# Kernel tuning notes

Measured on AMD Instinct MI355X. Metric: run time of the kernel, lower is better.

The kernel has to match this reference:

```python
import jax, jax.numpy as jnp
import numpy as np

N_NODES = 10000
N_EDGES = 640000
D = 128
BN_EPS = 1e-5


def setup_inputs() -> dict:
    key = jax.random.key(0)
    k1, k2, k3 = jax.random.split(key, 3)
    x = jax.random.normal(k1, (N_NODES, D), dtype=jnp.float32)
    edge_index = jax.random.randint(k2, (2, N_EDGES), 0, N_NODES, dtype=jnp.int64)
    W = jax.random.normal(k3, (D, D), dtype=jnp.float32) * (1.0 / np.sqrt(D))
    b = jnp.zeros((D,), dtype=jnp.float32)
    gamma = jnp.ones((D,), dtype=jnp.float32)
    beta = jnp.zeros((D,), dtype=jnp.float32)
    return {"x": x, "edge_index": edge_index, "W": W, "b": b, "gamma": gamma, "beta": beta}


def reference(x, edge_index, W, b, gamma, beta):
    # GINConv: out_i = MLP((1+eps)*x_i + sum_{j->i} x_j), eps=0
    src = edge_index[0]
    dst = edge_index[1]
    agg = jax.ops.segment_sum(x[src], dst, num_segments=N_NODES)  # [N, D]
    h = agg + x  # (1 + eps) * x with eps = 0
    # MLP inside GINConv: Linear + ReLU
    h = jnp.maximum(h @ W + b, 0.0)
    # outer F.relu (idempotent after inner ReLU, kept for faithfulness)
    h = jnp.maximum(h, 0.0)
    # BatchNorm1d, training-mode batch statistics (biased variance)
    mean = jnp.mean(h, axis=0)
    var = jnp.var(h, axis=0)
    h = (h - mean) * jax.lax.rsqrt(var + BN_EPS) * gamma + beta
    # Dropout in eval mode -> identity. his_x = [h]; return the main output.
    return h
```

## Files before the change

### kernel.cpp

```cpp
#include <hip/hip_runtime.h>

#define N_NODES 10000
#define N_EDGES 640000
#define D 128
#define BN_EPS 1e-5f
#define CAP 128
#define NSTRIPE 16
#define RPB 8
#define NB 1250
#define NBC 157
#define BCAPC 4608
#define ABLK 256
#define ASLICE 2500
#define CSENT 1250

typedef _Float16 half8_t __attribute__((ext_vector_type(8)));
typedef float f32x4 __attribute__((ext_vector_type(4)));
typedef unsigned short u16;

__global__ __launch_bounds__(256) void k_bin(
    const int* __restrict__ ei,
    const float4* __restrict__ x4,
    int* cur,
    int* __restrict__ recs,
    half8_t* __restrict__ xh)
{
    __shared__ int cnt[NBC];
    __shared__ int base_[NBC];
    __shared__ int loff[NBC];
    __shared__ int sc[256];
    __shared__ int sorted[ASLICE];
    const int b = blockIdx.x, t = threadIdx.x;

    {
        const int n8 = N_NODES * D / 8;
        for (int i = b * 256 + t; i < n8; i += ABLK * 256) {
            const float4 a = x4[2 * i];
            const float4 c = x4[2 * i + 1];
            half8_t h;
            h[0] = (_Float16)a.x; h[1] = (_Float16)a.y;
            h[2] = (_Float16)a.z; h[3] = (_Float16)a.w;
            h[4] = (_Float16)c.x; h[5] = (_Float16)c.y;
            h[6] = (_Float16)c.z; h[7] = (_Float16)c.w;
            xh[i] = h;
        }
    }

    if (t < NBC) cnt[t] = 0;
    __syncthreads();

    const int e0 = b * ASLICE;
    for (int i = t; i < ASLICE; i += 256)
        atomicAdd(&cnt[ei[N_EDGES + e0 + i] >> 6], 1);
    __syncthreads();

    sc[t] = (t < NBC) ? cnt[t] : 0;
    __syncthreads();
    #pragma unroll
    for (int off = 1; off < 256; off <<= 1) {
        const int add = (t >= off) ? sc[t - off] : 0;
        __syncthreads();
        sc[t] += add;
        __syncthreads();
    }

    const unsigned cbase = (unsigned)cur[CSENT];
    if (t < NBC) {
        loff[t]  = sc[t] - cnt[t];
        base_[t] = (int)((unsigned)atomicAdd(&cur[t], cnt[t]) - cbase);
        cnt[t]   = 0;
    }
    __syncthreads();

    for (int i = t; i < ASLICE; i += 256) {
        const int e = e0 + i;
        const int d = ei[N_EDGES + e];
        const int s = ei[e];
        const int bin = d >> 6;
        const int p = atomicAdd(&cnt[bin], 1);
        sorted[loff[bin] + p] = (s << 6) | (d & 63);
    }
    __syncthreads();

    const int g = t >> 4, sl = t & 15;
    for (int bin = g; bin < NBC; bin += 16) {
        const int c  = cnt[bin];
        const int gb = base_[bin];
        const int lo = loff[bin];
        for (int k = sl; k < c; k += 16) {
            const int pos = gb + k;
            if (pos < BCAPC) recs[bin * BCAPC + pos] = sorted[lo + k];
        }
    }
}

__global__ __launch_bounds__(256) void k_gfill(
    const float* __restrict__ x,
    const half8_t* __restrict__ xh8,
    const int* __restrict__ cur,
    const int* __restrict__ recs,
    const float* __restrict__ W,
    const float* __restrict__ bias,
    float* __restrict__ out,
    float* __restrict__ stats)
{
    __shared__ u16 lst[RPB * CAP];
    __shared__ int cnt[RPB];
    __shared__ float hs[RPB][D];
    const int tid  = threadIdx.x;
    const int bin  = blockIdx.x;
    const int cb   = bin >> 3;
    const int sub  = bin & 7;
    const int wv   = tid >> 6;
    const int lane = tid & 63;
    const int qq   = lane >> 4;
    const int l    = lane & 15;
    const float4* __restrict__ x4 = (const float4*)x;

    if (tid < RPB) cnt[tid] = 0;
    __syncthreads();

    const unsigned cbase = (unsigned)cur[CSENT];
    int nrec = (int)((unsigned)cur[cb] - cbase);
    if (nrec > BCAPC) nrec = BCAPC;
    const int* __restrict__ br = recs + cb * BCAPC;
    for (int i = tid; i < nrec; i += 256) {
        const int r = br[i];
        if (((r >> 3) & 7) == sub) {
            const int p = atomicAdd(&cnt[r & 7], 1);
            if (p < CAP) lst[(r & 7) * CAP + p] = (u16)(r >> 6);
        }
    }
    __syncthreads();

    #pragma unroll
    for (int j = 0; j < 2; j++) {
        const int lrow = wv * 2 + j;
        const int node = bin * RPB + lrow;
        int n = cnt[lrow];
        if (n > CAP) n = CAP;
        const u16* __restrict__ myl = &lst[lrow * CAP];
        float acc[8];
        #pragma unroll
        for (int z = 0; z < 8; z++) acc[z] = 0.f;

        int i = 0;
        for (; i + 64 <= n; i += 64) {
            const int sj = (int)myl[i + lane];
            #pragma unroll
            for (int b = 0; b < 2; b++) {
                half8_t v[8];
                #pragma unroll
                for (int u = 0; u < 8; u++) {
                    const int s = __shfl(sj, 4 * (b * 8 + u) + qq, 64);
                    v[u] = xh8[(size_t)s * 16 + l];
                }
                #pragma unroll
                for (int u = 0; u < 8; u++)
                    #pragma unroll
                    for (int z = 0; z < 8; z++)
                        acc[z] += (float)v[u][z];
            }
        }
        const int c = n - i;
        if (c > 0) {
            const int sj = (lane < c) ? (int)myl[i + lane] : 0;
            const int quads = c >> 2;
            for (int t2 = 0; t2 < quads; t2 += 8) {
                half8_t v[8];
                #pragma unroll
                for (int u = 0; u < 8; u++) {
                    const int s = __shfl(sj, (4 * (t2 + u) + qq) & 63, 64);
                    v[u] = xh8[(size_t)s * 16 + l];
                }
                #pragma unroll
                for (int u = 0; u < 8; u++) {
                    if (t2 + u < quads) {
                        #pragma unroll
                        for (int z = 0; z < 8; z++)
                            acc[z] += (float)v[u][z];
                    }
                }
            }
            const int r = c & 3;
            if (r > 0) {
                const int s = __shfl(sj, (4 * quads + qq) & 63, 64);
                const half8_t vv = xh8[(size_t)s * 16 + l];
                if (qq < r) {
                    #pragma unroll
                    for (int z = 0; z < 8; z++)
                        acc[z] += (float)vv[z];
                }
            }
        }
        #pragma unroll
        for (int z = 0; z < 8; z++) {
            acc[z] += __shfl_xor(acc[z], 16, 64);
            acc[z] += __shfl_xor(acc[z], 32, 64);
        }
        if (qq == 0) {
            const float4 xa = x4[(size_t)node * 32 + 2 * l];
            const float4 xb = x4[(size_t)node * 32 + 2 * l + 1];
            *(float4*)&hs[lrow][8 * l] =
                make_float4(acc[0] + xa.x, acc[1] + xa.y, acc[2] + xa.z, acc[3] + xa.w);
            *(float4*)&hs[lrow][8 * l + 4] =
                make_float4(acc[4] + xb.x, acc[5] + xb.y, acc[6] + xb.z, acc[7] + xb.w);
        }
    }
    __syncthreads();

    const int col = tid & 127;
    const int rg  = tid >> 7;
    float a[4] = {0.f, 0.f, 0.f, 0.f};
    #pragma unroll 8
    for (int k = 0; k < D; k++) {
        const float w = W[k * D + col];
        #pragma unroll
        for (int r = 0; r < 4; r++)
            a[r] = fmaf(hs[rg * 4 + r][k], w, a[r]);
    }

    const float bcol = bias[col];
    float s1 = 0.f, s2 = 0.f;
    #pragma unroll
    for (int r = 0; r < 4; r++) {
        const float v = fmaxf(a[r] + bcol, 0.f);
        __builtin_nontemporal_store(v, &out[(size_t)(bin * RPB + rg * 4 + r) * D + col]);
        s1 += v;
        s2 += v * v;
    }

    __syncthreads();
    float* red = &hs[0][0];
    red[tid]       = s1;
    red[256 + tid] = s2;
    __syncthreads();
    if (tid < D) {
        float* sp = &stats[(size_t)(bin & (NSTRIPE - 1)) * 256];
        atomicAdd(&sp[tid],     red[tid]       + red[tid + 128]);
        atomicAdd(&sp[D + tid], red[256 + tid] + red[256 + tid + 128]);
    }
}

__global__ __launch_bounds__(256) void k_bn(
    float* out,
    const float* __restrict__ stats,
    const float* __restrict__ gamma,
    const float* __restrict__ beta)
{
    __shared__ float sc[D], sh[D];
    const int tid = threadIdx.x;
    if (tid < D) {
        const float fbase = stats[NSTRIPE * 256];
        float s = 0.f, q = 0.f;
        #pragma unroll
        for (int cp = 0; cp < NSTRIPE; cp++) {
            s += stats[cp * 256 + tid]     - fbase;
            q += stats[cp * 256 + D + tid] - fbase;
        }
        const float mean = s * (1.0f / N_NODES);
        const float var  = q * (1.0f / N_NODES) - mean * mean;
        const float scale = gamma[tid] * rsqrtf(var + BN_EPS);
        sc[tid] = scale;
        sh[tid] = beta[tid] - mean * scale;
    }
    __syncthreads();

    f32x4* o4 = (f32x4*)out;
    #pragma unroll
    for (int j = 0; j < 2; j++) {
        const int f = blockIdx.x * 512 + j * 256 + tid;
        const int c = (f & 31) << 2;
        f32x4 v = __builtin_nontemporal_load(&o4[f]);
        v.x = v.x * sc[c]     + sh[c];
        v.y = v.y * sc[c + 1] + sh[c + 1];
        v.z = v.z * sc[c + 2] + sh[c + 2];
        v.w = v.w * sc[c + 3] + sh[c + 3];
        __builtin_nontemporal_store(v, &o4[f]);
    }
}

extern "C" void kernel_launch(void* const* d_in, const int* in_sizes, int n_in,
                              void* d_out, int out_size, void* d_ws, size_t ws_size,
                              hipStream_t stream)
{
    const float* x     = (const float*)d_in[0];
    const int*   ei    = (const int*)d_in[1];
    const float* W     = (const float*)d_in[2];
    const float* bias  = (const float*)d_in[3];
    const float* gamma = (const float*)d_in[4];
    const float* beta  = (const float*)d_in[5];
    float* out = (float*)d_out;

    float*   stats = (float*)d_ws;
    int*     cur   = (int*)(stats + NSTRIPE * 256 + 8);
    int*     recs  = cur + 1280;
    half8_t* xh    = (half8_t*)(recs + NBC * BCAPC);

    k_bin<<<ABLK, 256, 0, stream>>>(ei, (const float4*)x, cur, recs, xh);
    k_gfill<<<NB, 256, 0, stream>>>(x, xh, cur, recs, W, bias, out, stats);
    k_bn<<<N_NODES * D / 2048, 256, 0, stream>>>(out, stats, gamma, beta);
}
```

Baseline: 116.6 us.

## Replace global atomic bin cursors with fixed per-block record slots

The binning kernel no longer reserves space in each destination bin with a global atomicAdd on a shared cursor. Each (bin, source block) pair now writes into its own fixed-size slot and stores its count in a separate counts array. The gather kernel then has each of its 256 threads walk one source block's slot for its bin, instead of striding over one contiguous per-bin list. This removes contended global atomics and the cursor sentinel bookkeeping. In exchange, each slot is capped at 48 records, so an unusually dense bin from one slice would silently drop edges, and the per-thread serial slot reads are less coalesced.

New measurement: 166.9 us. +43.1%, slower.

```diff
diff --git a/kernel.cpp b/kernel.cpp
--- a/kernel.cpp
+++ b/kernel.cpp
@@ -9,10 +9,10 @@
 #define RPB 8
 #define NB 1250
 #define NBC 157
-#define BCAPC 4608
+#define SLOT 48
+#define CNTP 160
 #define ABLK 256
 #define ASLICE 2500
-#define CSENT 1250
 
 typedef _Float16 half8_t __attribute__((ext_vector_type(8)));
 typedef float f32x4 __attribute__((ext_vector_type(4)));
@@ -21,12 +21,11 @@
 __global__ __launch_bounds__(256) void k_bin(
     const int* __restrict__ ei,
     const float4* __restrict__ x4,
-    int* cur,
     int* __restrict__ recs,
+    int* __restrict__ cnts,
     half8_t* __restrict__ xh)
 {
     __shared__ int cnt[NBC];
-    __shared__ int base_[NBC];
     __shared__ int loff[NBC];
     __shared__ int sc[256];
     __shared__ int sorted[ASLICE];
@@ -64,12 +63,7 @@
         __syncthreads();
     }
 
-    const unsigned cbase = (unsigned)cur[CSENT];
-    if (t < NBC) {
-        loff[t]  = sc[t] - cnt[t];
-        base_[t] = (int)((unsigned)atomicAdd(&cur[t], cnt[t]) - cbase);
-        cnt[t]   = 0;
-    }
+    if (t < NBC) { loff[t] = sc[t] - cnt[t]; cnt[t] = 0; }
     __syncthreads();
 
     for (int i = t; i < ASLICE; i += 256) {
@@ -84,20 +78,18 @@
 
     const int g = t >> 4, sl = t & 15;
     for (int bin = g; bin < NBC; bin += 16) {
-        const int c  = cnt[bin];
-        const int gb = base_[bin];
+        int c = cnt[bin]; if (c > SLOT) c = SLOT;
+        int* __restrict__ dst = recs + (size_t)((bin << 8) + b) * SLOT;
         const int lo = loff[bin];
-        for (int k = sl; k < c; k += 16) {
-            const int pos = gb + k;
-            if (pos < BCAPC) recs[bin * BCAPC + pos] = sorted[lo + k];
-        }
-    }
+        for (int k = sl; k < c; k += 16) dst[k] = sorted[lo + k];
+    }
+    if (t < NBC) cnts[b * CNTP + t] = cnt[t];
 }
 
 __global__ __launch_bounds__(256) void k_gfill(
     const float* __restrict__ x,
     const half8_t* __restrict__ xh8,
-    const int* __restrict__ cur,
+    const int* __restrict__ cnts,
     const int* __restrict__ recs,
     const float* __restrict__ W,
     const float* __restrict__ bias,
@@ -120,15 +112,16 @@
     if (tid < RPB) cnt[tid] = 0;
     __syncthreads();
 
-    const unsigned cbase = (unsigned)cur[CSENT];
-    int nrec = (int)((unsigned)cur[cb] - cbase);
-    if (nrec > BCAPC) nrec = BCAPC;
-    const int* __restrict__ br = recs + cb * BCAPC;
-    for (int i = tid; i < nrec; i += 256) {
-        const int r = br[i];
-        if (((r >> 3) & 7) == sub) {
-            const int p = atomicAdd(&cnt[r & 7], 1);
-            if (p < CAP) lst[(r & 7) * CAP + p] = (u16)(r >> 6);
+    {
+        int c = cnts[tid * CNTP + cb];
+        if (c > SLOT) c = SLOT;
+        const int* __restrict__ seg = recs + (size_t)((cb << 8) + tid) * SLOT;
+        for (int k = 0; k < c; k++) {
+            const int r = seg[k];
+            if (((r >> 3) & 7) == sub) {
+                const int p = atomicAdd(&cnt[r & 7], 1);
+                if (p < CAP) lst[(r & 7) * CAP + p] = (u16)(r >> 6);
+            }
         }
     }
     __syncthreads();
@@ -248,7 +241,7 @@
     const float* __restrict__ gamma,
     const float* __restrict__ beta)
 {
-    __shared__ float sc[D], sh[D];
+    __shared__ float sc_[D], sh[D];
     const int tid = threadIdx.x;
     if (tid < D) {
         const float fbase = stats[NSTRIPE * 256];
@@ -261,7 +254,7 @@
         const float mean = s * (1.0f / N_NODES);
         const float var  = q * (1.0f / N_NODES) - mean * mean;
         const float scale = gamma[tid] * rsqrtf(var + BN_EPS);
-        sc[tid] = scale;
+        sc_[tid] = scale;
         sh[tid] = beta[tid] - mean * scale;
     }
     __syncthreads();
@@ -272,10 +265,10 @@
         const int f = blockIdx.x * 512 + j * 256 + tid;
         const int c = (f & 31) << 2;
         f32x4 v = __builtin_nontemporal_load(&o4[f]);
-        v.x = v.x * sc[c]     + sh[c];
-        v.y = v.y * sc[c + 1] + sh[c + 1];
-        v.z = v.z * sc[c + 2] + sh[c + 2];
-        v.w = v.w * sc[c + 3] + sh[c + 3];
+        v.x = v.x * sc_[c]     + sh[c];
+        v.y = v.y * sc_[c + 1] + sh[c + 1];
+        v.z = v.z * sc_[c + 2] + sh[c + 2];
+        v.w = v.w * sc_[c + 3] + sh[c + 3];
         __builtin_nontemporal_store(v, &o4[f]);
     }
 }
@@ -293,11 +286,11 @@
     float* out = (float*)d_out;
 
     float*   stats = (float*)d_ws;
-    int*     cur   = (int*)(stats + NSTRIPE * 256 + 8);
-    int*     recs  = cur + 1280;
-    half8_t* xh    = (half8_t*)(recs + NBC * BCAPC);
-
-    k_bin<<<ABLK, 256, 0, stream>>>(ei, (const float4*)x, cur, recs, xh);
-    k_gfill<<<NB, 256, 0, stream>>>(x, xh, cur, recs, W, bias, out, stats);
+    int*     cnts  = (int*)(stats + NSTRIPE * 256 + 8);
+    int*     recs  = cnts + 256 * CNTP;
+    half8_t* xh    = (half8_t*)(recs + (size_t)NBC * 256 * SLOT);
+
+    k_bin<<<ABLK, 256, 0, stream>>>(ei, (const float4*)x, recs, cnts, xh);
+    k_gfill<<<NB, 256, 0, stream>>>(x, xh, cnts, recs, W, bias, out, stats);
     k_bn<<<N_NODES * D / 2048, 256, 0, stream>>>(out, stats, gamma, beta);
 }
```
